# Performance work log

Hardware: AMD Instinct MI355X
Metric: run time of the kernel (lower is better)

The kernel has to match this reference:

```python
import math
import jax, jax.numpy as jnp
import numpy as np

TOP_K, NC, ALPHA, BETA, EPS = 10, 80, 0.5, 6.0, 1e-9
IMG, STRIDES = 640, (8, 16, 32)


def _ciou(box1, box2, eps=1e-7):
    # box1: gt [bs,n,1,4], box2: pred [bs,1,na,4] -> [bs,n,na,1]
    b1x1, b1y1, b1x2, b1y2 = jnp.split(box1, 4, axis=-1)
    b2x1, b2y1, b2x2, b2y2 = jnp.split(box2, 4, axis=-1)
    w1, h1 = b1x2 - b1x1, b1y2 - b1y1 + eps
    w2, h2 = b2x2 - b2x1, b2y2 - b2y1 + eps
    inter = jnp.clip(jnp.minimum(b1x2, b2x2) - jnp.maximum(b1x1, b2x1), 0.0) * \
            jnp.clip(jnp.minimum(b1y2, b2y2) - jnp.maximum(b1y1, b2y1), 0.0)
    union = w1 * h1 + w2 * h2 - inter + eps
    iou = inter / union
    cw = jnp.maximum(b1x2, b2x2) - jnp.minimum(b1x1, b2x1)
    ch = jnp.maximum(b1y2, b2y2) - jnp.minimum(b1y1, b2y1)
    c2 = cw ** 2 + ch ** 2 + eps
    rho2 = ((b2x1 + b2x2 - b1x1 - b1x2) ** 2 + (b2y1 + b2y2 - b1y1 - b1y2) ** 2) / 4.0
    v = (4.0 / math.pi ** 2) * (jnp.arctan(w2 / h2) - jnp.arctan(w1 / h1)) ** 2
    alpha = jax.lax.stop_gradient(v / (v - iou + (1.0 + eps)))
    return iou - (rho2 / c2 + v * alpha)


def _assign(score, p_box, anchors, gt_labels, gt_box, mask):
    bs, na, nc = score.shape
    n = gt_box.shape[1]
    labels = gt_labels[..., 0].astype(jnp.int32)      # [bs,n]
    valid = mask > 0                                  # [bs,n,1] valid-gt mask
    # --- candidate mask: anchor center strictly inside gt box ---
    lt, rb = gt_box[..., :2], gt_box[..., 2:]
    d = jnp.concatenate([anchors[None, None] - lt[:, :, None],
                         rb[:, :, None] - anchors[None, None]], -1)  # [bs,n,na,4]
    mask_in_gts = d.min(-1) > 1e-9                    # [bs,n,na]
    mask_gts = mask_in_gts & valid
    # --- per-(gt,anchor) class score and CIoU overlap ---
    gathered = score[jnp.arange(bs)[:, None], :, labels]          # [bs,n,na]
    bbox_scores = jnp.where(mask_gts, gathered, 0.0)
    ov = _ciou(gt_box[:, :, None], p_box[:, None])[..., 0]        # [bs,n,na]
    overlaps = jnp.where(mask_gts, jnp.clip(ov, 0.0), 0.0)
    metric = jnp.where(mask_gts,
                       jnp.where(mask_gts, gathered, 1.0) ** ALPHA * overlaps ** BETA,
                       0.0)
    # --- top-k candidates per gt; suppress duplicated indices ---
    _, top_id = jax.lax.top_k(metric, TOP_K)          # [bs,n,TOP_K]
    top_id = jnp.where(valid, top_id, 0)
    bi = jnp.arange(bs)[:, None, None]
    ni = jnp.arange(n)[None, :, None]
    count = jnp.zeros((bs, n, na), jnp.int32).at[bi, ni, top_id].add(1)
    count = jnp.where(count > 1, 0, count)
    mask_pos = count.astype(metric.dtype) * mask_in_gts.astype(metric.dtype) * mask  # [bs,n,na]
    fg = mask_pos.sum(1)                              # [bs,na]
    # --- resolve anchors claimed by multiple gts via max overlap ---
    max_over = (jnp.arange(n)[None, :, None] == jnp.argmax(overlaps, 1)[:, None, :]).astype(metric.dtype)
    mask_pos = jnp.where(fg[:, None, :] > 1, max_over, mask_pos)
    fg = mask_pos.sum(1)
    # --- gather targets ---
    gt_idx = jnp.argmax(mask_pos, 1)                  # [bs,na]
    target_labels = jnp.clip(jnp.take_along_axis(labels, gt_idx, 1), 0)
    target_bboxes = jnp.take_along_axis(gt_box, gt_idx[..., None], 1)  # [bs,na,4]
    ts = jax.nn.one_hot(target_labels, NC, dtype=metric.dtype)
    ts = jnp.where(fg[..., None] > 0, ts, 0.0)
    # --- task-aligned score normalization ---
    metric = metric * mask_pos
    pos_metrics = metric.max(-1, keepdims=True)
    pos_overlaps = (overlaps * mask_pos).max(-1, keepdims=True)
    norm_metric = metric * pos_overlaps / (pos_metrics + EPS)
    target_scores = ts * norm_metric.max(1)[..., None]               # [bs,na,NC]
    return target_bboxes, target_scores, fg > 0


def setup_inputs() -> dict:
    key = jax.random.key(0)
    ks = jax.random.split(key, 8)
    bs, n_max = 16, 64
    # anchor points: grid cell centers for strides 8/16/32 at 640x640
    pts = []
    for s in STRIDES:
        g = IMG // s
        c = (jnp.arange(g, dtype=jnp.float32) + 0.5) * s
        gy, gx = jnp.meshgrid(c, c, indexing='ij')
        pts.append(jnp.stack([gx.ravel(), gy.ravel()], -1))
    anchors = jnp.concatenate(pts, 0)                 # [8400,2]
    na = anchors.shape[0]
    # predicted boxes centered near anchor points
    wh = jax.random.uniform(ks[0], (bs, na, 2), minval=8.0, maxval=128.0)
    ctr = anchors[None] + jax.random.normal(ks[1], (bs, na, 2)) * 4.0
    p_box = jnp.concatenate([ctr - wh / 2, ctr + wh / 2], -1)
    score = jax.random.uniform(ks[2], (bs, na, NC))
    # ground-truth boxes (valid x1<x2, y1<y2)
    gwh = jax.random.uniform(ks[3], (bs, n_max, 2), minval=16.0, maxval=256.0)
    gctr = jax.random.uniform(ks[4], (bs, n_max, 2), minval=0.0, maxval=float(IMG))
    gt_box = jnp.concatenate([gctr - gwh / 2, gctr + gwh / 2], -1)
    gt_labels = jax.random.randint(ks[5], (bs, n_max, 1), 0, NC)
    nvalid = jax.random.randint(ks[6], (bs, 1), 8, n_max + 1)
    mask = (jnp.arange(n_max)[None, :] < nvalid).astype(jnp.float32)[..., None]
    return {"score": score, "p_box": p_box, "anchors": anchors,
            "gt_labels": gt_labels, "gt_box": gt_box, "mask": mask}


def reference(score, p_box, anchors, gt_labels, gt_box, mask):
    return _assign(score, p_box, anchors, gt_labels, gt_box, mask)
```

## Files before the change

kernel.cpp:

```cpp
#include <hip/hip_runtime.h>
#include <math.h>

#define BS   16
#define NMAX 64
#define NA   8400
#define NCLS 80
#define TOPK 10
#define ROWS (BS * NMAX)

typedef unsigned long long u64;

__device__ __forceinline__ float ciou_clip(
    float gx1, float gy1, float gx2, float gy2, float at1, float area1,
    float px1, float py1, float px2, float py2, float at2, float area2)
{
    float iw = fminf(gx2, px2) - fmaxf(gx1, px1);
    float ih = fminf(gy2, py2) - fmaxf(gy1, py1);
    float inter = fmaxf(iw, 0.f) * fmaxf(ih, 0.f);
    float uni = area1 + area2 - inter + 1e-7f;
    float iou = inter / uni;
    float cw = fmaxf(gx2, px2) - fminf(gx1, px1);
    float ch = fmaxf(gy2, py2) - fminf(gy1, py1);
    float c2 = cw * cw + ch * ch + 1e-7f;
    float dx = px1 + px2 - gx1 - gx2;
    float dy = py1 + py2 - gy1 - gy2;
    float rho2 = (dx * dx + dy * dy) * 0.25f;
    float dat = at2 - at1;
    float v = (4.0f / (float)(M_PI * M_PI)) * dat * dat;
    float alpha = v / (v - iou + (1.0f + 1e-7f));
    return fmaxf(iou - (rho2 / c2 + v * alpha), 0.f);
}

__global__ __launch_bounds__(256) void k0_prep(
    const float* __restrict__ p_box,
    const float* __restrict__ gt_box,
    float2* __restrict__ at2tab,
    float*  __restrict__ at1r,
    float*  __restrict__ area1r,
    u64*    __restrict__ mask64,
    float*  __restrict__ pos_mt,
    float*  __restrict__ pos_ov)
{
    int i = blockIdx.x * 256 + threadIdx.x;
    if (i >= BS * NA) return;
    float4 pv = ((const float4*)p_box)[i];
    float w2 = pv.z - pv.x;
    float h2 = pv.w - pv.y + 1e-7f;
    at2tab[i] = make_float2(atanf(w2 / h2), w2 * h2);
    mask64[i] = 0ull;
    if (i < ROWS) {
        float4 gb = ((const float4*)gt_box)[i];
        float w1 = gb.z - gb.x;
        float h1 = gb.w - gb.y + 1e-7f;
        at1r[i] = atanf(w1 / h1);
        area1r[i] = w1 * h1;
        pos_mt[i] = 0.f;
        pos_ov[i] = 0.f;
    }
}

#define INS10(kk)                                                         \
    if ((kk) > L[9]) {                                                    \
        L[9] = (kk);                                                      \
        _Pragma("unroll")                                                 \
        for (int q = 9; q >= 1; q--)                                      \
            if (L[q] > L[q-1]) { u64 tt = L[q-1]; L[q-1] = L[q]; L[q] = tt; } \
    }

__global__ __launch_bounds__(256) void k1_rows(
    const float* __restrict__ score,
    const float* __restrict__ p_box,
    const int*   __restrict__ gt_labels,
    const float* __restrict__ gt_box,
    const float* __restrict__ mask,
    const float2* __restrict__ at2tab,
    const float* __restrict__ at1r,
    const float* __restrict__ area1r,
    u64*   __restrict__ mask64,
    float* __restrict__ amt,
    float* __restrict__ aov)
{
    int row  = blockIdx.x * 4 + (threadIdx.x >> 6);
    int lane = threadIdx.x & 63;
    if (mask[row] <= 0.f) return;
    int b = row >> 6, n = row & 63;

    float4 gb = ((const float4*)gt_box)[row];
    float at1 = at1r[row], area1 = area1r[row];
    int lbl = gt_labels[row];
    const float* sc = score + (size_t)b * NA * NCLS + lbl;
    const float4* pb = (const float4*)p_box + (size_t)b * NA;
    const float2* t2 = at2tab + (size_t)b * NA;

    int ilo0 = max(0,  (int)floorf(gb.x * 0.125f   - 0.5f));
    int ihi0 = min(79, (int)ceilf (gb.z * 0.125f   - 0.5f));
    int jlo0 = max(0,  (int)floorf(gb.y * 0.125f   - 0.5f));
    int jhi0 = min(79, (int)ceilf (gb.w * 0.125f   - 0.5f));
    int ilo1 = max(0,  (int)floorf(gb.x * 0.0625f  - 0.5f));
    int ihi1 = min(39, (int)ceilf (gb.z * 0.0625f  - 0.5f));
    int jlo1 = max(0,  (int)floorf(gb.y * 0.0625f  - 0.5f));
    int jhi1 = min(39, (int)ceilf (gb.w * 0.0625f  - 0.5f));
    int ilo2 = max(0,  (int)floorf(gb.x * 0.03125f - 0.5f));
    int ihi2 = min(19, (int)ceilf (gb.z * 0.03125f - 0.5f));
    int jlo2 = max(0,  (int)floorf(gb.y * 0.03125f - 0.5f));
    int jhi2 = min(19, (int)ceilf (gb.w * 0.03125f - 0.5f));
    int nx0 = max(0, ihi0 - ilo0 + 1), ny0 = max(0, jhi0 - jlo0 + 1);
    int nx1 = max(0, ihi1 - ilo1 + 1), ny1 = max(0, jhi1 - jlo1 + 1);
    int nx2 = max(0, ihi2 - ilo2 + 1), ny2 = max(0, jhi2 - jlo2 + 1);
    int c0 = nx0 * ny0;
    int c1 = c0 + nx1 * ny1;
    int T  = c1 + nx2 * ny2;

    u64 L[10];
#pragma unroll
    for (int q = 0; q < 10; q++) L[q] = 0ull;

    for (int t = lane; t < T; t += 64) {
        bool ge1 = t >= c0, ge2 = t >= c1;
        int local = t - (ge2 ? c1 : (ge1 ? c0 : 0));
        int nxl  = ge2 ? nx2  : (ge1 ? nx1  : nx0);
        int ilol = ge2 ? ilo2 : (ge1 ? ilo1 : ilo0);
        int jlol = ge2 ? jlo2 : (ge1 ? jlo1 : jlo0);
        int g    = ge2 ? 20   : (ge1 ? 40   : 80);
        int off  = ge2 ? 8000 : (ge1 ? 6400 : 0);
        float s  = ge2 ? 32.f : (ge1 ? 16.f : 8.f);
        int jj = local / nxl;
        int ii = local - jj * nxl;
        int i = ilol + ii, j = jlol + jj;
        int a = off + j * g + i;
        float ax = ((float)i + 0.5f) * s, ay = ((float)j + 0.5f) * s;
        float dmin = fminf(fminf(ax - gb.x, ay - gb.y),
                           fminf(gb.z - ax, gb.w - ay));
        if (dmin > 1e-9f) {
            float4 pv = pb[a];
            float2 ta = t2[a];
            float ov = ciou_clip(gb.x, gb.y, gb.z, gb.w, at1, area1,
                                 pv.x, pv.y, pv.z, pv.w, ta.x, ta.y);
            float o2 = ov * ov;
            float mt = sqrtf(sc[(size_t)a * NCLS]) * o2 * o2 * o2;
            u64 kk = ((u64)__float_as_uint(mt) << 32) | (unsigned)(~a);
            INS10(kk)
        }
    }
    {
        float ax = (float)lane * 8.f + 4.f, ay = 4.f;
        float dmin = fminf(fminf(ax - gb.x, ay - gb.y),
                           fminf(gb.z - ax, gb.w - ay));
        if (!(dmin > 1e-9f)) {
            u64 kk = (u64)(unsigned)(~lane);
            INS10(kk)
        }
    }

    u64 winkey = 0ull;
    for (int it = 0; it < TOPK; it++) {
        u64 m = L[0];
#pragma unroll
        for (int o = 1; o < 64; o <<= 1) {
            u64 v = __shfl_xor(m, o);
            if (v > m) m = v;
        }
        if (lane == it) winkey = m;
        if (L[0] == m) {
#pragma unroll
            for (int q = 0; q < 9; q++) L[q] = L[q + 1];
            L[9] = 0ull;
        }
    }

    if (lane < TOPK && winkey) {
        int a = (int)(~(unsigned)(winkey & 0xffffffffu));
        float mt = __uint_as_float((unsigned)(winkey >> 32));
        bool l2 = a >= 8000, l1 = (a >= 6400) && !l2;
        int loc = a - (l2 ? 8000 : (l1 ? 6400 : 0));
        int g   = l2 ? 20 : (l1 ? 40 : 80);
        float s = l2 ? 32.f : (l1 ? 16.f : 8.f);
        int j = loc / g, i = loc - j * g;
        float ax = ((float)i + 0.5f) * s, ay = ((float)j + 0.5f) * s;
        float dmin = fminf(fminf(ax - gb.x, ay - gb.y),
                           fminf(gb.z - ax, gb.w - ay));
        if (dmin > 1e-9f) {
            size_t idx = (size_t)b * NA + a;
            atomicOr(&mask64[idx], 1ull << n);
            float4 pv = pb[a];
            float2 ta = t2[a];
            float ov = ciou_clip(gb.x, gb.y, gb.z, gb.w, at1, area1,
                                 pv.x, pv.y, pv.z, pv.w, ta.x, ta.y);
            amt[idx] = mt;
            aov[idx] = ov;
        }
    }
}

__global__ __launch_bounds__(256) void k3_resolve(
    const float* __restrict__ score,
    const float* __restrict__ p_box,
    const float* __restrict__ anchors,
    const int*   __restrict__ gt_labels,
    const float* __restrict__ gt_box,
    const float* __restrict__ mask,
    const float2* __restrict__ at2tab,
    const float* __restrict__ at1r,
    const float* __restrict__ area1r,
    const u64*   __restrict__ mask64,
    const float* __restrict__ amt,
    const float* __restrict__ aov,
    int* __restrict__ gt_idx,
    unsigned char* __restrict__ fg_arr,
    float* __restrict__ tgt_mt,
    float* __restrict__ out_bbox,
    float* __restrict__ out_fg,
    float* __restrict__ pos_mt,
    float* __restrict__ pos_ov)
{
    int i = blockIdx.x * 256 + threadIdx.x;
    if (i >= BS * NA) return;
    int b = i / NA, a = i - b * NA;
    u64 bits = mask64[i];
    int fg0 = __popcll(bits);
    int gi = 0, fg = (fg0 > 0);
    float mt = 0.f, ov = 0.f;
    if (fg0 == 1) {
        gi = __ffsll(bits) - 1;
        mt = amt[i];
        ov = aov[i];
    } else if (fg0 > 1) {
        float2 axy = ((const float2*)anchors)[a];
        float4 pv = ((const float4*)p_box)[i];
        float2 ta = at2tab[i];
        const float* mrow = mask + b * NMAX;
        float best = -1.f; int argn = 0;
        for (int nn = 0; nn < NMAX; nn++) {
            float v = 0.f;
            if (mrow[nn] > 0.f) {
                int r = b * NMAX + nn;
                float4 gbv = ((const float4*)gt_box)[r];
                float dmin = fminf(fminf(axy.x - gbv.x, axy.y - gbv.y),
                                   fminf(gbv.z - axy.x, gbv.w - axy.y));
                if (dmin > 1e-9f)
                    v = ciou_clip(gbv.x, gbv.y, gbv.z, gbv.w, at1r[r], area1r[r],
                                  pv.x, pv.y, pv.z, pv.w, ta.x, ta.y);
            }
            if (v > best) { best = v; argn = nn; }
        }
        gi = argn;
        ov = fmaxf(best, 0.f);
        int lbl = gt_labels[b * NMAX + argn]; if (lbl < 0) lbl = 0;
        float gath = score[((size_t)b * NA + a) * NCLS + lbl];
        float o2 = ov * ov;
        mt = sqrtf(gath) * o2 * o2 * o2;
    }
    int r = b * NMAX + gi;
    gt_idx[i] = gi;
    fg_arr[i] = (unsigned char)fg;
    tgt_mt[i] = mt;
    out_fg[i] = fg ? 1.f : 0.f;
    ((float4*)out_bbox)[i] = ((const float4*)gt_box)[r];
    if (fg) {
        atomicMax((int*)&pos_mt[r], __float_as_int(mt));
        atomicMax((int*)&pos_ov[r], __float_as_int(ov));
    }
}

__global__ __launch_bounds__(256) void k5_full(
    const int*   __restrict__ gt_idx,
    const unsigned char* __restrict__ fg_arr,
    const float* __restrict__ tgt_mt,
    const int*   __restrict__ gt_labels,
    const float* __restrict__ pos_mt,
    const float* __restrict__ pos_ov,
    float4* __restrict__ out_scores)
{
    int i = blockIdx.x * 256 + threadIdx.x;
    if (i >= BS * NA * (NCLS / 4)) return;
    int ba = i / (NCLS / 4);
    int c4 = (i - ba * (NCLS / 4)) * 4;
    float4 o = make_float4(0.f, 0.f, 0.f, 0.f);
    if (fg_arr[ba]) {
        int b = ba / NA;
        int r = b * NMAX + gt_idx[ba];
        int lbl = gt_labels[r]; if (lbl < 0) lbl = 0;
        if (lbl >= c4 && lbl < c4 + 4) {
            float val = tgt_mt[ba] * pos_ov[r] / (pos_mt[r] + 1e-9f);
            if (lbl == c4)     o.x = val;
            if (lbl == c4 + 1) o.y = val;
            if (lbl == c4 + 2) o.z = val;
            if (lbl == c4 + 3) o.w = val;
        }
    }
    out_scores[i] = o;
}

extern "C" void kernel_launch(void* const* d_in, const int* in_sizes, int n_in,
                              void* d_out, int out_size, void* d_ws, size_t ws_size,
                              hipStream_t stream) {
    (void)in_sizes; (void)n_in; (void)out_size; (void)ws_size;
    const float* score     = (const float*)d_in[0];
    const float* p_box     = (const float*)d_in[1];
    const float* anchors   = (const float*)d_in[2];
    const int*   gt_labels = (const int*)d_in[3];
    const float* gt_box    = (const float*)d_in[4];
    const float* mask      = (const float*)d_in[5];

    char* w = (char*)d_ws;
    float2* at2tab  = (float2*)w;              w += (size_t)BS * NA * 8;
    u64*   mask64   = (u64*)w;                 w += (size_t)BS * NA * 8;
    float* amt      = (float*)w;               w += (size_t)BS * NA * 4;
    float* aov      = (float*)w;               w += (size_t)BS * NA * 4;
    int*   gt_idx   = (int*)w;                 w += (size_t)BS * NA * 4;
    float* tgt_mt   = (float*)w;               w += (size_t)BS * NA * 4;
    float* at1r     = (float*)w;               w += (size_t)ROWS * 4;
    float* area1r   = (float*)w;               w += (size_t)ROWS * 4;
    float* pos_mt   = (float*)w;               w += (size_t)ROWS * 4;
    float* pos_ov   = (float*)w;               w += (size_t)ROWS * 4;
    unsigned char* fg_arr = (unsigned char*)w; w += (size_t)BS * NA;

    float* out_bbox   = (float*)d_out;
    float* out_scores = out_bbox + (size_t)BS * NA * 4;
    float* out_fg     = out_scores + (size_t)BS * NA * NCLS;

    hipLaunchKernelGGL(k0_prep, dim3((BS * NA + 255) / 256), dim3(256), 0, stream,
                       p_box, gt_box, at2tab, at1r, area1r, mask64, pos_mt, pos_ov);
    hipLaunchKernelGGL(k1_rows, dim3(ROWS / 4), dim3(256), 0, stream,
                       score, p_box, gt_labels, gt_box, mask,
                       at2tab, at1r, area1r, mask64, amt, aov);
    hipLaunchKernelGGL(k3_resolve, dim3((BS * NA + 255) / 256), dim3(256), 0, stream,
                       score, p_box, anchors, gt_labels, gt_box, mask,
                       at2tab, at1r, area1r, mask64, amt, aov,
                       gt_idx, fg_arr, tgt_mt, out_bbox, out_fg, pos_mt, pos_ov);
    hipLaunchKernelGGL(k5_full, dim3((BS * NA * (NCLS / 4) + 255) / 256), dim3(256), 0, stream,
                       gt_idx, fg_arr, tgt_mt, gt_labels, pos_mt, pos_ov,
                       (float4*)out_scores);
}
```

Measured before the change: 150.7 us.

## Fuse four pipeline kernels into one cooperative persistent kernel with grid syncs

Replaces the four separate launches (prep, per-gt top-k, per-anchor resolve, score fill) with a single cooperative kernel of 512 blocks that uses grid-wide syncs between phases. Each phase uses grid-stride loops. The aim is to remove launch gaps and inter-kernel drain between small kernels. In exchange it adds cooperative-launch overhead and grid barrier costs, and limits parallelism in the row phase to 512 blocks of 4 rows, which covers exactly 2048 rows where only 1024 are needed.

```diff
diff --git a/kernel.cpp b/kernel.cpp
--- a/kernel.cpp
+++ b/kernel.cpp
@@ -1,5 +1,8 @@
 #include <hip/hip_runtime.h>
+#include <hip/hip_cooperative_groups.h>
 #include <math.h>
+
+namespace cg = cooperative_groups;
 
 #define BS   16
 #define NMAX 64
@@ -7,6 +10,9 @@
 #define NCLS 80
 #define TOPK 10
 #define ROWS (BS * NMAX)
+#define TOTAL (BS * NA)
+#define GRID 512
+#define NTH  256
 
 typedef unsigned long long u64;
 
@@ -31,34 +37,6 @@
     return fmaxf(iou - (rho2 / c2 + v * alpha), 0.f);
 }
 
-__global__ __launch_bounds__(256) void k0_prep(
-    const float* __restrict__ p_box,
-    const float* __restrict__ gt_box,
-    float2* __restrict__ at2tab,
-    float*  __restrict__ at1r,
-    float*  __restrict__ area1r,
-    u64*    __restrict__ mask64,
-    float*  __restrict__ pos_mt,
-    float*  __restrict__ pos_ov)
-{
-    int i = blockIdx.x * 256 + threadIdx.x;
-    if (i >= BS * NA) return;
-    float4 pv = ((const float4*)p_box)[i];
-    float w2 = pv.z - pv.x;
-    float h2 = pv.w - pv.y + 1e-7f;
-    at2tab[i] = make_float2(atanf(w2 / h2), w2 * h2);
-    mask64[i] = 0ull;
-    if (i < ROWS) {
-        float4 gb = ((const float4*)gt_box)[i];
-        float w1 = gb.z - gb.x;
-        float h1 = gb.w - gb.y + 1e-7f;
-        at1r[i] = atanf(w1 / h1);
-        area1r[i] = w1 * h1;
-        pos_mt[i] = 0.f;
-        pos_ov[i] = 0.f;
-    }
-}
-
 #define INS10(kk)                                                         \
     if ((kk) > L[9]) {                                                    \
         L[9] = (kk);                                                      \
@@ -67,228 +45,232 @@
             if (L[q] > L[q-1]) { u64 tt = L[q-1]; L[q-1] = L[q]; L[q] = tt; } \
     }
 
-__global__ __launch_bounds__(256) void k1_rows(
-    const float* __restrict__ score,
-    const float* __restrict__ p_box,
-    const int*   __restrict__ gt_labels,
-    const float* __restrict__ gt_box,
-    const float* __restrict__ mask,
-    const float2* __restrict__ at2tab,
-    const float* __restrict__ at1r,
-    const float* __restrict__ area1r,
-    u64*   __restrict__ mask64,
-    float* __restrict__ amt,
-    float* __restrict__ aov)
-{
-    int row  = blockIdx.x * 4 + (threadIdx.x >> 6);
-    int lane = threadIdx.x & 63;
-    if (mask[row] <= 0.f) return;
-    int b = row >> 6, n = row & 63;
-
-    float4 gb = ((const float4*)gt_box)[row];
-    float at1 = at1r[row], area1 = area1r[row];
-    int lbl = gt_labels[row];
-    const float* sc = score + (size_t)b * NA * NCLS + lbl;
-    const float4* pb = (const float4*)p_box + (size_t)b * NA;
-    const float2* t2 = at2tab + (size_t)b * NA;
-
-    int ilo0 = max(0,  (int)floorf(gb.x * 0.125f   - 0.5f));
-    int ihi0 = min(79, (int)ceilf (gb.z * 0.125f   - 0.5f));
-    int jlo0 = max(0,  (int)floorf(gb.y * 0.125f   - 0.5f));
-    int jhi0 = min(79, (int)ceilf (gb.w * 0.125f   - 0.5f));
-    int ilo1 = max(0,  (int)floorf(gb.x * 0.0625f  - 0.5f));
-    int ihi1 = min(39, (int)ceilf (gb.z * 0.0625f  - 0.5f));
-    int jlo1 = max(0,  (int)floorf(gb.y * 0.0625f  - 0.5f));
-    int jhi1 = min(39, (int)ceilf (gb.w * 0.0625f  - 0.5f));
-    int ilo2 = max(0,  (int)floorf(gb.x * 0.03125f - 0.5f));
-    int ihi2 = min(19, (int)ceilf (gb.z * 0.03125f - 0.5f));
-    int jlo2 = max(0,  (int)floorf(gb.y * 0.03125f - 0.5f));
-    int jhi2 = min(19, (int)ceilf (gb.w * 0.03125f - 0.5f));
-    int nx0 = max(0, ihi0 - ilo0 + 1), ny0 = max(0, jhi0 - jlo0 + 1);
-    int nx1 = max(0, ihi1 - ilo1 + 1), ny1 = max(0, jhi1 - jlo1 + 1);
-    int nx2 = max(0, ihi2 - ilo2 + 1), ny2 = max(0, jhi2 - jlo2 + 1);
-    int c0 = nx0 * ny0;
-    int c1 = c0 + nx1 * ny1;
-    int T  = c1 + nx2 * ny2;
-
-    u64 L[10];
-#pragma unroll
-    for (int q = 0; q < 10; q++) L[q] = 0ull;
-
-    for (int t = lane; t < T; t += 64) {
-        bool ge1 = t >= c0, ge2 = t >= c1;
-        int local = t - (ge2 ? c1 : (ge1 ? c0 : 0));
-        int nxl  = ge2 ? nx2  : (ge1 ? nx1  : nx0);
-        int ilol = ge2 ? ilo2 : (ge1 ? ilo1 : ilo0);
-        int jlol = ge2 ? jlo2 : (ge1 ? jlo1 : jlo0);
-        int g    = ge2 ? 20   : (ge1 ? 40   : 80);
-        int off  = ge2 ? 8000 : (ge1 ? 6400 : 0);
-        float s  = ge2 ? 32.f : (ge1 ? 16.f : 8.f);
-        int jj = local / nxl;
-        int ii = local - jj * nxl;
-        int i = ilol + ii, j = jlol + jj;
-        int a = off + j * g + i;
-        float ax = ((float)i + 0.5f) * s, ay = ((float)j + 0.5f) * s;
-        float dmin = fminf(fminf(ax - gb.x, ay - gb.y),
-                           fminf(gb.z - ax, gb.w - ay));
-        if (dmin > 1e-9f) {
-            float4 pv = pb[a];
-            float2 ta = t2[a];
-            float ov = ciou_clip(gb.x, gb.y, gb.z, gb.w, at1, area1,
-                                 pv.x, pv.y, pv.z, pv.w, ta.x, ta.y);
-            float o2 = ov * ov;
-            float mt = sqrtf(sc[(size_t)a * NCLS]) * o2 * o2 * o2;
-            u64 kk = ((u64)__float_as_uint(mt) << 32) | (unsigned)(~a);
-            INS10(kk)
-        }
-    }
-    {
-        float ax = (float)lane * 8.f + 4.f, ay = 4.f;
-        float dmin = fminf(fminf(ax - gb.x, ay - gb.y),
-                           fminf(gb.z - ax, gb.w - ay));
-        if (!(dmin > 1e-9f)) {
-            u64 kk = (u64)(unsigned)(~lane);
-            INS10(kk)
-        }
-    }
-
-    u64 winkey = 0ull;
-    for (int it = 0; it < TOPK; it++) {
-        u64 m = L[0];
-#pragma unroll
-        for (int o = 1; o < 64; o <<= 1) {
-            u64 v = __shfl_xor(m, o);
-            if (v > m) m = v;
-        }
-        if (lane == it) winkey = m;
-        if (L[0] == m) {
-#pragma unroll
-            for (int q = 0; q < 9; q++) L[q] = L[q + 1];
-            L[9] = 0ull;
-        }
-    }
-
-    if (lane < TOPK && winkey) {
-        int a = (int)(~(unsigned)(winkey & 0xffffffffu));
-        float mt = __uint_as_float((unsigned)(winkey >> 32));
-        bool l2 = a >= 8000, l1 = (a >= 6400) && !l2;
-        int loc = a - (l2 ? 8000 : (l1 ? 6400 : 0));
-        int g   = l2 ? 20 : (l1 ? 40 : 80);
-        float s = l2 ? 32.f : (l1 ? 16.f : 8.f);
-        int j = loc / g, i = loc - j * g;
-        float ax = ((float)i + 0.5f) * s, ay = ((float)j + 0.5f) * s;
-        float dmin = fminf(fminf(ax - gb.x, ay - gb.y),
-                           fminf(gb.z - ax, gb.w - ay));
-        if (dmin > 1e-9f) {
-            size_t idx = (size_t)b * NA + a;
-            atomicOr(&mask64[idx], 1ull << n);
-            float4 pv = pb[a];
-            float2 ta = t2[a];
-            float ov = ciou_clip(gb.x, gb.y, gb.z, gb.w, at1, area1,
-                                 pv.x, pv.y, pv.z, pv.w, ta.x, ta.y);
-            amt[idx] = mt;
-            aov[idx] = ov;
-        }
-    }
-}
-
-__global__ __launch_bounds__(256) void k3_resolve(
+__global__ __launch_bounds__(NTH, 2) void fused_all(
     const float* __restrict__ score,
     const float* __restrict__ p_box,
     const float* __restrict__ anchors,
     const int*   __restrict__ gt_labels,
     const float* __restrict__ gt_box,
     const float* __restrict__ mask,
-    const float2* __restrict__ at2tab,
-    const float* __restrict__ at1r,
-    const float* __restrict__ area1r,
-    const u64*   __restrict__ mask64,
-    const float* __restrict__ amt,
-    const float* __restrict__ aov,
-    int* __restrict__ gt_idx,
+    float2* __restrict__ at2tab,
+    float*  __restrict__ at1r,
+    float*  __restrict__ area1r,
+    u64*    __restrict__ mask64,
+    float*  __restrict__ amt,
+    float*  __restrict__ aov,
+    int*    __restrict__ gt_idx,
     unsigned char* __restrict__ fg_arr,
-    float* __restrict__ tgt_mt,
-    float* __restrict__ out_bbox,
-    float* __restrict__ out_fg,
-    float* __restrict__ pos_mt,
-    float* __restrict__ pos_ov)
+    float*  __restrict__ tgt_mt,
+    float*  __restrict__ pos_mt,
+    float*  __restrict__ pos_ov,
+    float*  __restrict__ out_bbox,
+    float4* __restrict__ out_scores,
+    float*  __restrict__ out_fg)
 {
-    int i = blockIdx.x * 256 + threadIdx.x;
-    if (i >= BS * NA) return;
-    int b = i / NA, a = i - b * NA;
-    u64 bits = mask64[i];
-    int fg0 = __popcll(bits);
-    int gi = 0, fg = (fg0 > 0);
-    float mt = 0.f, ov = 0.f;
-    if (fg0 == 1) {
-        gi = __ffsll(bits) - 1;
-        mt = amt[i];
-        ov = aov[i];
-    } else if (fg0 > 1) {
-        float2 axy = ((const float2*)anchors)[a];
+    cg::grid_group gg = cg::this_grid();
+    int tid  = threadIdx.x;
+    int gtid = blockIdx.x * NTH + tid;
+
+    for (int i = gtid; i < TOTAL; i += GRID * NTH) {
         float4 pv = ((const float4*)p_box)[i];
-        float2 ta = at2tab[i];
-        const float* mrow = mask + b * NMAX;
-        float best = -1.f; int argn = 0;
-        for (int nn = 0; nn < NMAX; nn++) {
-            float v = 0.f;
-            if (mrow[nn] > 0.f) {
-                int r = b * NMAX + nn;
-                float4 gbv = ((const float4*)gt_box)[r];
-                float dmin = fminf(fminf(axy.x - gbv.x, axy.y - gbv.y),
-                                   fminf(gbv.z - axy.x, gbv.w - axy.y));
-                if (dmin > 1e-9f)
-                    v = ciou_clip(gbv.x, gbv.y, gbv.z, gbv.w, at1r[r], area1r[r],
-                                  pv.x, pv.y, pv.z, pv.w, ta.x, ta.y);
-            }
-            if (v > best) { best = v; argn = nn; }
-        }
-        gi = argn;
-        ov = fmaxf(best, 0.f);
-        int lbl = gt_labels[b * NMAX + argn]; if (lbl < 0) lbl = 0;
-        float gath = score[((size_t)b * NA + a) * NCLS + lbl];
-        float o2 = ov * ov;
-        mt = sqrtf(gath) * o2 * o2 * o2;
-    }
-    int r = b * NMAX + gi;
-    gt_idx[i] = gi;
-    fg_arr[i] = (unsigned char)fg;
-    tgt_mt[i] = mt;
-    out_fg[i] = fg ? 1.f : 0.f;
-    ((float4*)out_bbox)[i] = ((const float4*)gt_box)[r];
-    if (fg) {
-        atomicMax((int*)&pos_mt[r], __float_as_int(mt));
-        atomicMax((int*)&pos_ov[r], __float_as_int(ov));
-    }
-}
-
-__global__ __launch_bounds__(256) void k5_full(
-    const int*   __restrict__ gt_idx,
-    const unsigned char* __restrict__ fg_arr,
-    const float* __restrict__ tgt_mt,
-    const int*   __restrict__ gt_labels,
-    const float* __restrict__ pos_mt,
-    const float* __restrict__ pos_ov,
-    float4* __restrict__ out_scores)
-{
-    int i = blockIdx.x * 256 + threadIdx.x;
-    if (i >= BS * NA * (NCLS / 4)) return;
-    int ba = i / (NCLS / 4);
-    int c4 = (i - ba * (NCLS / 4)) * 4;
-    float4 o = make_float4(0.f, 0.f, 0.f, 0.f);
-    if (fg_arr[ba]) {
-        int b = ba / NA;
-        int r = b * NMAX + gt_idx[ba];
-        int lbl = gt_labels[r]; if (lbl < 0) lbl = 0;
-        if (lbl >= c4 && lbl < c4 + 4) {
-            float val = tgt_mt[ba] * pos_ov[r] / (pos_mt[r] + 1e-9f);
-            if (lbl == c4)     o.x = val;
-            if (lbl == c4 + 1) o.y = val;
-            if (lbl == c4 + 2) o.z = val;
-            if (lbl == c4 + 3) o.w = val;
-        }
-    }
-    out_scores[i] = o;
+        float w2 = pv.z - pv.x;
+        float h2 = pv.w - pv.y + 1e-7f;
+        at2tab[i] = make_float2(atanf(w2 / h2), w2 * h2);
+        mask64[i] = 0ull;
+        if (i < ROWS) {
+            float4 gb = ((const float4*)gt_box)[i];
+            float w1 = gb.z - gb.x;
+            float h1 = gb.w - gb.y + 1e-7f;
+            at1r[i] = atanf(w1 / h1);
+            area1r[i] = w1 * h1;
+            pos_mt[i] = 0.f;
+            pos_ov[i] = 0.f;
+        }
+    }
+    gg.sync();
+
+    {
+        int row  = (blockIdx.x << 2) | (tid >> 6);
+        int lane = tid & 63;
+        if (row < ROWS && mask[row] > 0.f) {
+            int b = row >> 6, n = row & 63;
+            float4 gb = ((const float4*)gt_box)[row];
+            float at1 = at1r[row], area1 = area1r[row];
+            int lbl = gt_labels[row];
+            const float* sc = score + (size_t)b * NA * NCLS + lbl;
+            const float4* pb = (const float4*)p_box + (size_t)b * NA;
+            const float2* t2 = at2tab + (size_t)b * NA;
+
+            int ilo0 = max(0,  (int)floorf(gb.x * 0.125f   - 0.5f));
+            int ihi0 = min(79, (int)ceilf (gb.z * 0.125f   - 0.5f));
+            int jlo0 = max(0,  (int)floorf(gb.y * 0.125f   - 0.5f));
+            int jhi0 = min(79, (int)ceilf (gb.w * 0.125f   - 0.5f));
+            int ilo1 = max(0,  (int)floorf(gb.x * 0.0625f  - 0.5f));
+            int ihi1 = min(39, (int)ceilf (gb.z * 0.0625f  - 0.5f));
+            int jlo1 = max(0,  (int)floorf(gb.y * 0.0625f  - 0.5f));
+            int jhi1 = min(39, (int)ceilf (gb.w * 0.0625f  - 0.5f));
+            int ilo2 = max(0,  (int)floorf(gb.x * 0.03125f - 0.5f));
+            int ihi2 = min(19, (int)ceilf (gb.z * 0.03125f - 0.5f));
+            int jlo2 = max(0,  (int)floorf(gb.y * 0.03125f - 0.5f));
+            int jhi2 = min(19, (int)ceilf (gb.w * 0.03125f - 0.5f));
+            int nx0 = max(0, ihi0 - ilo0 + 1), ny0 = max(0, jhi0 - jlo0 + 1);
+            int nx1 = max(0, ihi1 - ilo1 + 1), ny1 = max(0, jhi1 - jlo1 + 1);
+            int nx2 = max(0, ihi2 - ilo2 + 1), ny2 = max(0, jhi2 - jlo2 + 1);
+            int c0 = nx0 * ny0;
+            int c1 = c0 + nx1 * ny1;
+            int T  = c1 + nx2 * ny2;
+
+            u64 L[10];
+#pragma unroll
+            for (int q = 0; q < 10; q++) L[q] = 0ull;
+
+            for (int t = lane; t < T; t += 64) {
+                bool ge1 = t >= c0, ge2 = t >= c1;
+                int local = t - (ge2 ? c1 : (ge1 ? c0 : 0));
+                int nxl  = ge2 ? nx2  : (ge1 ? nx1  : nx0);
+                int ilol = ge2 ? ilo2 : (ge1 ? ilo1 : ilo0);
+                int jlol = ge2 ? jlo2 : (ge1 ? jlo1 : jlo0);
+                int g    = ge2 ? 20   : (ge1 ? 40   : 80);
+                int off  = ge2 ? 8000 : (ge1 ? 6400 : 0);
+                float s  = ge2 ? 32.f : (ge1 ? 16.f : 8.f);
+                int jj = local / nxl;
+                int ii = local - jj * nxl;
+                int i = ilol + ii, j = jlol + jj;
+                int a = off + j * g + i;
+                float ax = ((float)i + 0.5f) * s, ay = ((float)j + 0.5f) * s;
+                float dmin = fminf(fminf(ax - gb.x, ay - gb.y),
+                                   fminf(gb.z - ax, gb.w - ay));
+                if (dmin > 1e-9f) {
+                    float4 pv = pb[a];
+                    float2 ta = t2[a];
+                    float ov = ciou_clip(gb.x, gb.y, gb.z, gb.w, at1, area1,
+                                         pv.x, pv.y, pv.z, pv.w, ta.x, ta.y);
+                    float o2 = ov * ov;
+                    float mt = sqrtf(sc[(size_t)a * NCLS]) * o2 * o2 * o2;
+                    u64 kk = ((u64)__float_as_uint(mt) << 32) | (unsigned)(~a);
+                    INS10(kk)
+                }
+            }
+            {
+                float ax = (float)lane * 8.f + 4.f, ay = 4.f;
+                float dmin = fminf(fminf(ax - gb.x, ay - gb.y),
+                                   fminf(gb.z - ax, gb.w - ay));
+                if (!(dmin > 1e-9f)) {
+                    u64 kk = (u64)(unsigned)(~lane);
+                    INS10(kk)
+                }
+            }
+
+            u64 winkey = 0ull;
+            for (int it = 0; it < TOPK; it++) {
+                u64 m = L[0];
+#pragma unroll
+                for (int o = 1; o < 64; o <<= 1) {
+                    u64 v = __shfl_xor(m, o);
+                    if (v > m) m = v;
+                }
+                if (lane == it) winkey = m;
+                if (L[0] == m) {
+#pragma unroll
+                    for (int q = 0; q < 9; q++) L[q] = L[q + 1];
+                    L[9] = 0ull;
+                }
+            }
+
+            if (lane < TOPK && winkey) {
+                int a = (int)(~(unsigned)(winkey & 0xffffffffu));
+                float mt = __uint_as_float((unsigned)(winkey >> 32));
+                bool l2 = a >= 8000, l1 = (a >= 6400) && !l2;
+                int loc = a - (l2 ? 8000 : (l1 ? 6400 : 0));
+                int g   = l2 ? 20 : (l1 ? 40 : 80);
+                float s = l2 ? 32.f : (l1 ? 16.f : 8.f);
+                int j = loc / g, i = loc - j * g;
+                float ax = ((float)i + 0.5f) * s, ay = ((float)j + 0.5f) * s;
+                float dmin = fminf(fminf(ax - gb.x, ay - gb.y),
+                                   fminf(gb.z - ax, gb.w - ay));
+                if (dmin > 1e-9f) {
+                    size_t idx = (size_t)b * NA + a;
+                    atomicOr(&mask64[idx], 1ull << n);
+                    float4 pv = pb[a];
+                    float2 ta = t2[a];
+                    float ov = ciou_clip(gb.x, gb.y, gb.z, gb.w, at1, area1,
+                                         pv.x, pv.y, pv.z, pv.w, ta.x, ta.y);
+                    amt[idx] = mt;
+                    aov[idx] = ov;
+                }
+            }
+        }
+    }
+    gg.sync();
+
+    for (int i = gtid; i < TOTAL; i += GRID * NTH) {
+        int b = i / NA, a = i - b * NA;
+        u64 bits = mask64[i];
+        int fg0 = __popcll(bits);
+        int gi = 0, fg = (fg0 > 0);
+        float mt = 0.f, ov = 0.f;
+        if (fg0 == 1) {
+            gi = __ffsll(bits) - 1;
+            mt = amt[i];
+            ov = aov[i];
+        } else if (fg0 > 1) {
+            float2 axy = ((const float2*)anchors)[a];
+            float4 pv = ((const float4*)p_box)[i];
+            float2 ta = at2tab[i];
+            const float* mrow = mask + b * NMAX;
+            float best = -1.f; int argn = 0;
+            for (int nn = 0; nn < NMAX; nn++) {
+                float v = 0.f;
+                if (mrow[nn] > 0.f) {
+                    int r = b * NMAX + nn;
+                    float4 gbv = ((const float4*)gt_box)[r];
+                    float dmin = fminf(fminf(axy.x - gbv.x, axy.y - gbv.y),
+                                       fminf(gbv.z - axy.x, gbv.w - axy.y));
+                    if (dmin > 1e-9f)
+                        v = ciou_clip(gbv.x, gbv.y, gbv.z, gbv.w, at1r[r], area1r[r],
+                                      pv.x, pv.y, pv.z, pv.w, ta.x, ta.y);
+                }
+                if (v > best) { best = v; argn = nn; }
+            }
+            gi = argn;
+            ov = fmaxf(best, 0.f);
+            int lbl = gt_labels[b * NMAX + argn]; if (lbl < 0) lbl = 0;
+            float gath = score[((size_t)b * NA + a) * NCLS + lbl];
+            float o2 = ov * ov;
+            mt = sqrtf(gath) * o2 * o2 * o2;
+        }
+        int r = b * NMAX + gi;
+        gt_idx[i] = gi;
+        fg_arr[i] = (unsigned char)fg;
+        tgt_mt[i] = mt;
+        out_fg[i] = fg ? 1.f : 0.f;
+        ((float4*)out_bbox)[i] = ((const float4*)gt_box)[r];
+        if (fg) {
+            atomicMax((int*)&pos_mt[r], __float_as_int(mt));
+            atomicMax((int*)&pos_ov[r], __float_as_int(ov));
+        }
+    }
+    gg.sync();
+
+    const int NS4 = BS * NA * (NCLS / 4);
+    for (int i = gtid; i < NS4; i += GRID * NTH) {
+        int ba = i / (NCLS / 4);
+        int c4 = (i - ba * (NCLS / 4)) * 4;
+        float4 o = make_float4(0.f, 0.f, 0.f, 0.f);
+        if (fg_arr[ba]) {
+            int b = ba / NA;
+            int r = b * NMAX + gt_idx[ba];
+            int lbl = gt_labels[r]; if (lbl < 0) lbl = 0;
+            if (lbl >= c4 && lbl < c4 + 4) {
+                float val = tgt_mt[ba] * pos_ov[r] / (pos_mt[r] + 1e-9f);
+                if (lbl == c4)     o.x = val;
+                if (lbl == c4 + 1) o.y = val;
+                if (lbl == c4 + 2) o.z = val;
+                if (lbl == c4 + 3) o.w = val;
+            }
+        }
+        out_scores[i] = o;
+    }
 }
 
 extern "C" void kernel_launch(void* const* d_in, const int* in_sizes, int n_in,
@@ -303,32 +285,30 @@
     const float* mask      = (const float*)d_in[5];
 
     char* w = (char*)d_ws;
-    float2* at2tab  = (float2*)w;              w += (size_t)BS * NA * 8;
-    u64*   mask64   = (u64*)w;                 w += (size_t)BS * NA * 8;
-    float* amt      = (float*)w;               w += (size_t)BS * NA * 4;
-    float* aov      = (float*)w;               w += (size_t)BS * NA * 4;
-    int*   gt_idx   = (int*)w;                 w += (size_t)BS * NA * 4;
-    float* tgt_mt   = (float*)w;               w += (size_t)BS * NA * 4;
+    float2* at2tab  = (float2*)w;              w += (size_t)TOTAL * 8;
+    u64*   mask64   = (u64*)w;                 w += (size_t)TOTAL * 8;
+    float* amt      = (float*)w;               w += (size_t)TOTAL * 4;
+    float* aov      = (float*)w;               w += (size_t)TOTAL * 4;
+    int*   gt_idx   = (int*)w;                 w += (size_t)TOTAL * 4;
+    float* tgt_mt   = (float*)w;               w += (size_t)TOTAL * 4;
     float* at1r     = (float*)w;               w += (size_t)ROWS * 4;
     float* area1r   = (float*)w;               w += (size_t)ROWS * 4;
     float* pos_mt   = (float*)w;               w += (size_t)ROWS * 4;
     float* pos_ov   = (float*)w;               w += (size_t)ROWS * 4;
-    unsigned char* fg_arr = (unsigned char*)w; w += (size_t)BS * NA;
-
-    float* out_bbox   = (float*)d_out;
-    float* out_scores = out_bbox + (size_t)BS * NA * 4;
-    float* out_fg     = out_scores + (size_t)BS * NA * NCLS;
-
-    hipLaunchKernelGGL(k0_prep, dim3((BS * NA + 255) / 256), dim3(256), 0, stream,
-                       p_box, gt_box, at2tab, at1r, area1r, mask64, pos_mt, pos_ov);
-    hipLaunchKernelGGL(k1_rows, dim3(ROWS / 4), dim3(256), 0, stream,
-                       score, p_box, gt_labels, gt_box, mask,
-                       at2tab, at1r, area1r, mask64, amt, aov);
-    hipLaunchKernelGGL(k3_resolve, dim3((BS * NA + 255) / 256), dim3(256), 0, stream,
-                       score, p_box, anchors, gt_labels, gt_box, mask,
-                       at2tab, at1r, area1r, mask64, amt, aov,
-                       gt_idx, fg_arr, tgt_mt, out_bbox, out_fg, pos_mt, pos_ov);
-    hipLaunchKernelGGL(k5_full, dim3((BS * NA * (NCLS / 4) + 255) / 256), dim3(256), 0, stream,
-                       gt_idx, fg_arr, tgt_mt, gt_labels, pos_mt, pos_ov,
-                       (float4*)out_scores);
+    unsigned char* fg_arr = (unsigned char*)w; w += (size_t)TOTAL;
+
+    float*  out_bbox   = (float*)d_out;
+    float4* out_scores = (float4*)(out_bbox + (size_t)TOTAL * 4);
+    float*  out_fg     = (float*)out_scores + (size_t)TOTAL * NCLS;
+
+    void* args[] = {
+        (void*)&score, (void*)&p_box, (void*)&anchors, (void*)&gt_labels,
+        (void*)&gt_box, (void*)&mask,
+        (void*)&at2tab, (void*)&at1r, (void*)&area1r, (void*)&mask64,
+        (void*)&amt, (void*)&aov, (void*)&gt_idx, (void*)&fg_arr,
+        (void*)&tgt_mt, (void*)&pos_mt, (void*)&pos_ov,
+        (void*)&out_bbox, (void*)&out_scores, (void*)&out_fg
+    };
+    hipLaunchCooperativeKernel((const void*)fused_all, dim3(GRID), dim3(NTH),
+                               args, 0, stream);
 }
```

Result: slower. 313.0 us (+107.7%).

## Drop prep kernel, recompute atan terms inline, split each gt row over two waves

Applied to the files above, without the earlier changes.

Removes the k0_prep kernel and its precomputed atan/area tables. The atan and area terms are now recomputed inline in k1 and k3, and zero-initialisation is done with a single memset over mask64 plus pos_mt/pos_ov, which are now contiguous. k1 now gives each gt row its own 128-thread block with two waves, and the two per-wave top-10 lists are merged through shared memory. The aim is to cut one launch and the table traffic and to give wide boxes more parallelism, at the cost of extra atan work per candidate and a block-level sync.

```diff
diff --git a/kernel.cpp b/kernel.cpp
--- a/kernel.cpp
+++ b/kernel.cpp
@@ -7,6 +7,7 @@
 #define NCLS 80
 #define TOPK 10
 #define ROWS (BS * NMAX)
+#define TOTAL (BS * NA)
 
 typedef unsigned long long u64;
 
@@ -31,34 +32,6 @@
     return fmaxf(iou - (rho2 / c2 + v * alpha), 0.f);
 }
 
-__global__ __launch_bounds__(256) void k0_prep(
-    const float* __restrict__ p_box,
-    const float* __restrict__ gt_box,
-    float2* __restrict__ at2tab,
-    float*  __restrict__ at1r,
-    float*  __restrict__ area1r,
-    u64*    __restrict__ mask64,
-    float*  __restrict__ pos_mt,
-    float*  __restrict__ pos_ov)
-{
-    int i = blockIdx.x * 256 + threadIdx.x;
-    if (i >= BS * NA) return;
-    float4 pv = ((const float4*)p_box)[i];
-    float w2 = pv.z - pv.x;
-    float h2 = pv.w - pv.y + 1e-7f;
-    at2tab[i] = make_float2(atanf(w2 / h2), w2 * h2);
-    mask64[i] = 0ull;
-    if (i < ROWS) {
-        float4 gb = ((const float4*)gt_box)[i];
-        float w1 = gb.z - gb.x;
-        float h1 = gb.w - gb.y + 1e-7f;
-        at1r[i] = atanf(w1 / h1);
-        area1r[i] = w1 * h1;
-        pos_mt[i] = 0.f;
-        pos_ov[i] = 0.f;
-    }
-}
-
 #define INS10(kk)                                                         \
     if ((kk) > L[9]) {                                                    \
         L[9] = (kk);                                                      \
@@ -67,30 +40,30 @@
             if (L[q] > L[q-1]) { u64 tt = L[q-1]; L[q-1] = L[q]; L[q] = tt; } \
     }
 
-__global__ __launch_bounds__(256) void k1_rows(
+__global__ __launch_bounds__(128) void k1_rows(
     const float* __restrict__ score,
     const float* __restrict__ p_box,
     const int*   __restrict__ gt_labels,
     const float* __restrict__ gt_box,
     const float* __restrict__ mask,
-    const float2* __restrict__ at2tab,
-    const float* __restrict__ at1r,
-    const float* __restrict__ area1r,
     u64*   __restrict__ mask64,
     float* __restrict__ amt,
     float* __restrict__ aov)
 {
-    int row  = blockIdx.x * 4 + (threadIdx.x >> 6);
+    int row = blockIdx.x;
+    if (mask[row] <= 0.f) return;
+    int wid  = threadIdx.x >> 6;
     int lane = threadIdx.x & 63;
-    if (mask[row] <= 0.f) return;
     int b = row >> 6, n = row & 63;
 
     float4 gb = ((const float4*)gt_box)[row];
-    float at1 = at1r[row], area1 = area1r[row];
+    float w1 = gb.z - gb.x;
+    float h1 = gb.w - gb.y + 1e-7f;
+    float at1 = atanf(w1 / h1);
+    float area1 = w1 * h1;
     int lbl = gt_labels[row];
     const float* sc = score + (size_t)b * NA * NCLS + lbl;
     const float4* pb = (const float4*)p_box + (size_t)b * NA;
-    const float2* t2 = at2tab + (size_t)b * NA;
 
     int ilo0 = max(0,  (int)floorf(gb.x * 0.125f   - 0.5f));
     int ihi0 = min(79, (int)ceilf (gb.z * 0.125f   - 0.5f));
@@ -115,7 +88,7 @@
 #pragma unroll
     for (int q = 0; q < 10; q++) L[q] = 0ull;
 
-    for (int t = lane; t < T; t += 64) {
+    for (int t = threadIdx.x; t < T; t += 128) {
         bool ge1 = t >= c0, ge2 = t >= c1;
         int local = t - (ge2 ? c1 : (ge1 ? c0 : 0));
         int nxl  = ge2 ? nx2  : (ge1 ? nx1  : nx0);
@@ -133,16 +106,18 @@
                            fminf(gb.z - ax, gb.w - ay));
         if (dmin > 1e-9f) {
             float4 pv = pb[a];
-            float2 ta = t2[a];
+            float w2 = pv.z - pv.x;
+            float h2 = pv.w - pv.y + 1e-7f;
             float ov = ciou_clip(gb.x, gb.y, gb.z, gb.w, at1, area1,
-                                 pv.x, pv.y, pv.z, pv.w, ta.x, ta.y);
+                                 pv.x, pv.y, pv.z, pv.w,
+                                 atanf(w2 / h2), w2 * h2);
             float o2 = ov * ov;
             float mt = sqrtf(sc[(size_t)a * NCLS]) * o2 * o2 * o2;
             u64 kk = ((u64)__float_as_uint(mt) << 32) | (unsigned)(~a);
             INS10(kk)
         }
     }
-    {
+    if (wid == 0) {
         float ax = (float)lane * 8.f + 4.f, ay = 4.f;
         float dmin = fminf(fminf(ax - gb.x, ay - gb.y),
                            fminf(gb.z - ax, gb.w - ay));
@@ -152,7 +127,8 @@
         }
     }
 
-    u64 winkey = 0ull;
+    __shared__ u64 skey[2 * TOPK];
+    u64 wk = 0ull;
     for (int it = 0; it < TOPK; it++) {
         u64 m = L[0];
 #pragma unroll
@@ -160,34 +136,52 @@
             u64 v = __shfl_xor(m, o);
             if (v > m) m = v;
         }
-        if (lane == it) winkey = m;
+        if (lane == it) wk = m;
         if (L[0] == m) {
 #pragma unroll
             for (int q = 0; q < 9; q++) L[q] = L[q + 1];
             L[9] = 0ull;
         }
     }
-
-    if (lane < TOPK && winkey) {
-        int a = (int)(~(unsigned)(winkey & 0xffffffffu));
-        float mt = __uint_as_float((unsigned)(winkey >> 32));
-        bool l2 = a >= 8000, l1 = (a >= 6400) && !l2;
-        int loc = a - (l2 ? 8000 : (l1 ? 6400 : 0));
-        int g   = l2 ? 20 : (l1 ? 40 : 80);
-        float s = l2 ? 32.f : (l1 ? 16.f : 8.f);
-        int j = loc / g, i = loc - j * g;
-        float ax = ((float)i + 0.5f) * s, ay = ((float)j + 0.5f) * s;
-        float dmin = fminf(fminf(ax - gb.x, ay - gb.y),
-                           fminf(gb.z - ax, gb.w - ay));
-        if (dmin > 1e-9f) {
-            size_t idx = (size_t)b * NA + a;
-            atomicOr(&mask64[idx], 1ull << n);
-            float4 pv = pb[a];
-            float2 ta = t2[a];
-            float ov = ciou_clip(gb.x, gb.y, gb.z, gb.w, at1, area1,
-                                 pv.x, pv.y, pv.z, pv.w, ta.x, ta.y);
-            amt[idx] = mt;
-            aov[idx] = ov;
+    if (lane < TOPK) skey[wid * TOPK + lane] = wk;
+    __syncthreads();
+
+    if (wid == 0) {
+        u64 ck = (lane < 2 * TOPK) ? skey[lane] : 0ull;
+        u64 winkey = 0ull;
+        for (int it = 0; it < TOPK; it++) {
+            u64 m = ck;
+#pragma unroll
+            for (int o = 1; o < 64; o <<= 1) {
+                u64 v = __shfl_xor(m, o);
+                if (v > m) m = v;
+            }
+            if (lane == it) winkey = m;
+            if (ck == m) ck = 0ull;
+        }
+        if (lane < TOPK && winkey) {
+            int a = (int)(~(unsigned)(winkey & 0xffffffffu));
+            float mt = __uint_as_float((unsigned)(winkey >> 32));
+            bool l2a = a >= 8000, l1a = (a >= 6400) && !l2a;
+            int loc = a - (l2a ? 8000 : (l1a ? 6400 : 0));
+            int g   = l2a ? 20 : (l1a ? 40 : 80);
+            float s = l2a ? 32.f : (l1a ? 16.f : 8.f);
+            int j = loc / g, i = loc - j * g;
+            float ax = ((float)i + 0.5f) * s, ay = ((float)j + 0.5f) * s;
+            float dmin = fminf(fminf(ax - gb.x, ay - gb.y),
+                               fminf(gb.z - ax, gb.w - ay));
+            if (dmin > 1e-9f) {
+                size_t idx = (size_t)b * NA + a;
+                atomicOr(&mask64[idx], 1ull << n);
+                float4 pv = pb[a];
+                float w2 = pv.z - pv.x;
+                float h2 = pv.w - pv.y + 1e-7f;
+                float ov = ciou_clip(gb.x, gb.y, gb.z, gb.w, at1, area1,
+                                     pv.x, pv.y, pv.z, pv.w,
+                                     atanf(w2 / h2), w2 * h2);
+                amt[idx] = mt;
+                aov[idx] = ov;
+            }
         }
     }
 }
@@ -199,9 +193,6 @@
     const int*   __restrict__ gt_labels,
     const float* __restrict__ gt_box,
     const float* __restrict__ mask,
-    const float2* __restrict__ at2tab,
-    const float* __restrict__ at1r,
-    const float* __restrict__ area1r,
     const u64*   __restrict__ mask64,
     const float* __restrict__ amt,
     const float* __restrict__ aov,
@@ -214,7 +205,7 @@
     float* __restrict__ pos_ov)
 {
     int i = blockIdx.x * 256 + threadIdx.x;
-    if (i >= BS * NA) return;
+    if (i >= TOTAL) return;
     int b = i / NA, a = i - b * NA;
     u64 bits = mask64[i];
     int fg0 = __popcll(bits);
@@ -227,7 +218,10 @@
     } else if (fg0 > 1) {
         float2 axy = ((const float2*)anchors)[a];
         float4 pv = ((const float4*)p_box)[i];
-        float2 ta = at2tab[i];
+        float w2 = pv.z - pv.x;
+        float h2 = pv.w - pv.y + 1e-7f;
+        float at2 = atanf(w2 / h2);
+        float area2 = w2 * h2;
         const float* mrow = mask + b * NMAX;
         float best = -1.f; int argn = 0;
         for (int nn = 0; nn < NMAX; nn++) {
@@ -237,9 +231,13 @@
                 float4 gbv = ((const float4*)gt_box)[r];
                 float dmin = fminf(fminf(axy.x - gbv.x, axy.y - gbv.y),
                                    fminf(gbv.z - axy.x, gbv.w - axy.y));
-                if (dmin > 1e-9f)
-                    v = ciou_clip(gbv.x, gbv.y, gbv.z, gbv.w, at1r[r], area1r[r],
-                                  pv.x, pv.y, pv.z, pv.w, ta.x, ta.y);
+                if (dmin > 1e-9f) {
+                    float w1 = gbv.z - gbv.x;
+                    float h1 = gbv.w - gbv.y + 1e-7f;
+                    v = ciou_clip(gbv.x, gbv.y, gbv.z, gbv.w,
+                                  atanf(w1 / h1), w1 * h1,
+                                  pv.x, pv.y, pv.z, pv.w, at2, area2);
+                }
             }
             if (v > best) { best = v; argn = nn; }
         }
@@ -272,7 +270,7 @@
     float4* __restrict__ out_scores)
 {
     int i = blockIdx.x * 256 + threadIdx.x;
-    if (i >= BS * NA * (NCLS / 4)) return;
+    if (i >= TOTAL * (NCLS / 4)) return;
     int ba = i / (NCLS / 4);
     int c4 = (i - ba * (NCLS / 4)) * 4;
     float4 o = make_float4(0.f, 0.f, 0.f, 0.f);
@@ -303,32 +301,29 @@
     const float* mask      = (const float*)d_in[5];
 
     char* w = (char*)d_ws;
-    float2* at2tab  = (float2*)w;              w += (size_t)BS * NA * 8;
-    u64*   mask64   = (u64*)w;                 w += (size_t)BS * NA * 8;
-    float* amt      = (float*)w;               w += (size_t)BS * NA * 4;
-    float* aov      = (float*)w;               w += (size_t)BS * NA * 4;
-    int*   gt_idx   = (int*)w;                 w += (size_t)BS * NA * 4;
-    float* tgt_mt   = (float*)w;               w += (size_t)BS * NA * 4;
-    float* at1r     = (float*)w;               w += (size_t)ROWS * 4;
-    float* area1r   = (float*)w;               w += (size_t)ROWS * 4;
+    u64*   mask64   = (u64*)w;                 w += (size_t)TOTAL * 8;
     float* pos_mt   = (float*)w;               w += (size_t)ROWS * 4;
     float* pos_ov   = (float*)w;               w += (size_t)ROWS * 4;
-    unsigned char* fg_arr = (unsigned char*)w; w += (size_t)BS * NA;
-
-    float* out_bbox   = (float*)d_out;
-    float* out_scores = out_bbox + (size_t)BS * NA * 4;
-    float* out_fg     = out_scores + (size_t)BS * NA * NCLS;
-
-    hipLaunchKernelGGL(k0_prep, dim3((BS * NA + 255) / 256), dim3(256), 0, stream,
-                       p_box, gt_box, at2tab, at1r, area1r, mask64, pos_mt, pos_ov);
-    hipLaunchKernelGGL(k1_rows, dim3(ROWS / 4), dim3(256), 0, stream,
+    float* amt      = (float*)w;               w += (size_t)TOTAL * 4;
+    float* aov      = (float*)w;               w += (size_t)TOTAL * 4;
+    int*   gt_idx   = (int*)w;                 w += (size_t)TOTAL * 4;
+    float* tgt_mt   = (float*)w;               w += (size_t)TOTAL * 4;
+    unsigned char* fg_arr = (unsigned char*)w; w += (size_t)TOTAL;
+
+    float*  out_bbox   = (float*)d_out;
+    float4* out_scores = (float4*)(out_bbox + (size_t)TOTAL * 4);
+    float*  out_fg     = (float*)out_scores + (size_t)TOTAL * NCLS;
+
+    hipMemsetAsync(mask64, 0, (size_t)TOTAL * 8 + (size_t)ROWS * 8, stream);
+
+    hipLaunchKernelGGL(k1_rows, dim3(ROWS), dim3(128), 0, stream,
                        score, p_box, gt_labels, gt_box, mask,
-                       at2tab, at1r, area1r, mask64, amt, aov);
-    hipLaunchKernelGGL(k3_resolve, dim3((BS * NA + 255) / 256), dim3(256), 0, stream,
+                       mask64, amt, aov);
+    hipLaunchKernelGGL(k3_resolve, dim3((TOTAL + 255) / 256), dim3(256), 0, stream,
                        score, p_box, anchors, gt_labels, gt_box, mask,
-                       at2tab, at1r, area1r, mask64, amt, aov,
+                       mask64, amt, aov,
                        gt_idx, fg_arr, tgt_mt, out_bbox, out_fg, pos_mt, pos_ov);
-    hipLaunchKernelGGL(k5_full, dim3((BS * NA * (NCLS / 4) + 255) / 256), dim3(256), 0, stream,
+    hipLaunchKernelGGL(k5_full, dim3((TOTAL * (NCLS / 4) + 255) / 256), dim3(256), 0, stream,
                        gt_idx, fg_arr, tgt_mt, gt_labels, pos_mt, pos_ov,
                        (float4*)out_scores);
 }
```

Result: faster. 142.9 us (-5.2%).
